# Optimization experiments

Hardware: AMD Instinct MI355X
Metric: run time of the kernel (lower is better)

Reference implementation:

```python
import jax, jax.numpy as jnp
import numpy as np

N_NODES = 50000
N_EDGES = 800000
F_DIM = 64


def setup_inputs() -> dict:
    key = jax.random.key(0)
    ks = jax.random.split(key, 8)
    idx_i = jax.random.randint(ks[0], (N_EDGES,), 0, N_NODES)
    idx_j = jax.random.randint(ks[1], (N_EDGES,), 0, N_NODES)
    px = jax.random.normal(ks[2], (N_NODES, 3, F_DIM), dtype=jnp.float32)
    diff = jax.random.normal(ks[3], (N_EDGES, 3, 1), dtype=jnp.float32)
    s = 1.0 / np.sqrt(F_DIM)
    W_pp = jax.random.normal(ks[4], (F_DIM, F_DIM), dtype=jnp.float32) * s
    W_i = jax.random.normal(ks[5], (F_DIM, F_DIM), dtype=jnp.float32) * s
    W_j = jax.random.normal(ks[6], (F_DIM, F_DIM), dtype=jnp.float32) * s
    W_ii = jax.random.normal(ks[7], (F_DIM, F_DIM), dtype=jnp.float32) * s
    return {"idx_i": idx_i, "idx_j": idx_j, "px": px, "diff": diff,
            "W_pp": W_pp, "W_i": W_i, "W_j": W_j, "W_ii": W_ii}


def reference(idx_i, idx_j, px, diff, W_pp, W_i, W_j, W_ii):
    # PPLayer: bias-free linear on feature dim. px: [N, 3, F]
    px1 = jnp.einsum('nvf,gf->nvg', px, W_pp)
    # PIXLayer: gather endpoints, two bias-free linears, sum. [E, 3, F]
    ix = (jnp.einsum('evf,gf->evg', px1[idx_i], W_i)
          + jnp.einsum('evf,gf->evg', px1[idx_j], W_j))
    # ScaleLayer: elementwise scale by per-edge direction. diff: [E, 3, 1]
    ix = ix * diff
    # IILayer: bias-free linear on edge messages
    ix = jnp.einsum('evf,gf->evg', ix, W_ii)
    # IPLayer: scatter_add back to nodes along dim 0
    px_out = jax.ops.segment_sum(ix, idx_i, num_segments=N_NODES)
    return (px_out, ix)
```

## Files before the change

### kernel.cpp

```cpp
#include <hip/hip_runtime.h>

#define N_NODES 50000
#define N_EDGES 800000
#define F 64
#define NROWS (N_NODES * 3)
#define NPX (N_NODES * 3 * F)

typedef float floatx4 __attribute__((ext_vector_type(4)));

__device__ __forceinline__ unsigned short f2bf(float f) {
  unsigned int u = __float_as_uint(f);
  return (unsigned short)((u + 0x7FFFu + ((u >> 16) & 1u)) >> 16);
}
__device__ __forceinline__ float bf2f(unsigned short h) {
  return __uint_as_float(((unsigned int)h) << 16);
}

__global__ __launch_bounds__(256) void mm64_pair(
    const float* __restrict__ A0, const float* __restrict__ B0, float* __restrict__ O0,
    const float* __restrict__ A1, const float* __restrict__ B1, float* __restrict__ O1) {
  const float* A = (blockIdx.x == 0) ? A0 : A1;
  const float* B = (blockIdx.x == 0) ? B0 : B1;
  float* O = (blockIdx.x == 0) ? O0 : O1;
  __shared__ float As[64][65];
  __shared__ float Bs[64][65];
  int t = threadIdx.x;
  for (int k = 0; k < 16; ++k) {
    int idx = t + 256 * k;
    As[idx >> 6][idx & 63] = A[idx];
    Bs[idx >> 6][idx & 63] = B[idx];
  }
  __syncthreads();
  int g = t >> 2, f0 = (t & 3) * 16;
  float acc[16];
  #pragma unroll
  for (int j = 0; j < 16; ++j) acc[j] = 0.f;
  for (int k = 0; k < 64; ++k) {
    float a = As[g][k];
    #pragma unroll
    for (int j = 0; j < 16; ++j) acc[j] += a * Bs[k][f0 + j];
  }
  for (int j = 0; j < 16; ++j) O[g * 64 + f0 + j] = acc[j];
}

__global__ __launch_bounds__(256) void node_mm(
    const float* __restrict__ px, const float* __restrict__ Bi,
    const float* __restrict__ Bj, float* __restrict__ yi,
    unsigned short* __restrict__ yjb) {
  __shared__ float pxs[64][68];
  __shared__ float Bs[128][68];
  int t = threadIdx.x;
  int r0 = blockIdx.x * 64;
  #pragma unroll
  for (int k = 0; k < 8; ++k) {
    int idx = t + 256 * k;
    int row = idx >> 4, c4 = (idx & 15) * 4;
    const float* src = (row < 64) ? (Bi + row * 64 + c4) : (Bj + (row - 64) * 64 + c4);
    *(float4*)&Bs[row][c4] = *(const float4*)src;
  }
  #pragma unroll
  for (int k = 0; k < 4; ++k) {
    int idx = t + 256 * k;
    int lr = idx >> 4, c4 = (idx & 15) * 4;
    float4 v = make_float4(0.f, 0.f, 0.f, 0.f);
    if (r0 + lr < NROWS) v = *(const float4*)(px + (size_t)(r0 + lr) * 64 + c4);
    *(float4*)&pxs[lr][c4] = v;
  }
  __syncthreads();
  int q = t & 31;
  int rg = t >> 5;
  float acc[8][4];
  #pragma unroll
  for (int r = 0; r < 8; ++r)
    #pragma unroll
    for (int j = 0; j < 4; ++j) acc[r][j] = 0.f;
  #pragma unroll 4
  for (int fc = 0; fc < 16; ++fc) {
    float4 b[4];
    #pragma unroll
    for (int j = 0; j < 4; ++j) b[j] = *(const float4*)&Bs[4 * q + j][fc * 4];
    #pragma unroll
    for (int r = 0; r < 8; ++r) {
      float4 p = *(const float4*)&pxs[rg * 8 + r][fc * 4];
      #pragma unroll
      for (int j = 0; j < 4; ++j)
        acc[r][j] += p.x * b[j].x + p.y * b[j].y + p.z * b[j].z + p.w * b[j].w;
    }
  }
  #pragma unroll
  for (int r = 0; r < 8; ++r) {
    int grow = r0 + rg * 8 + r;
    if (grow >= NROWS) continue;
    if (q < 16) {
      float4 v = make_float4(acc[r][0], acc[r][1], acc[r][2], acc[r][3]);
      *(float4*)(yi + (size_t)grow * 64 + q * 4) = v;
    } else {
      ushort4 h;
      h.x = f2bf(acc[r][0]); h.y = f2bf(acc[r][1]);
      h.z = f2bf(acc[r][2]); h.w = f2bf(acc[r][3]);
      *(ushort4*)(yjb + (size_t)grow * 64 + (q - 16) * 4) = h;
    }
  }
}

__global__ __launch_bounds__(256) void hist_kernel(
    const int* __restrict__ idx_i, int* __restrict__ cnt) {
  int e = blockIdx.x * 256 + threadIdx.x;
  if (e < N_EDGES) atomicAdd(&cnt[idx_i[e]], 1);
}

__global__ __launch_bounds__(1024) void scan_kernel(
    const int* __restrict__ cnt, int* __restrict__ offs, int* __restrict__ cursor) {
  __shared__ int wsum[16];
  __shared__ int s_carry;
  int t = threadIdx.x, w = t >> 6, l = t & 63;
  if (t == 0) { s_carry = 0; offs[0] = 0; }
  __syncthreads();
  for (int base = 0; base < N_NODES; base += 8192) {
    int i0 = base + t * 8;
    int x[8];
    if (i0 + 7 < N_NODES) {
      int4 a = *(const int4*)(cnt + i0);
      int4 b = *(const int4*)(cnt + i0 + 4);
      x[0] = a.x; x[1] = a.y; x[2] = a.z; x[3] = a.w;
      x[4] = b.x; x[5] = b.y; x[6] = b.z; x[7] = b.w;
    } else {
      #pragma unroll
      for (int k = 0; k < 8; ++k) x[k] = (i0 + k < N_NODES) ? cnt[i0 + k] : 0;
    }
    int incl[8];
    int p = 0;
    #pragma unroll
    for (int k = 0; k < 8; ++k) { p += x[k]; incl[k] = p; }
    int tsum = p;
    int ts = tsum;
    #pragma unroll
    for (int off = 1; off < 64; off <<= 1) {
      int y = __shfl_up(ts, off, 64);
      if (l >= off) ts += y;
    }
    if (l == 63) wsum[w] = ts;
    __syncthreads();
    if (t < 16) {
      int ws_ = wsum[t];
      int si = ws_;
      #pragma unroll
      for (int off = 1; off < 16; off <<= 1) {
        int y = __shfl_up(si, off, 16);
        if (t >= off) si += y;
      }
      wsum[t] = si - ws_;
    }
    __syncthreads();
    int basev = s_carry + wsum[w] + (ts - tsum);
    #pragma unroll
    for (int k = 0; k < 8; ++k) {
      int i = i0 + k;
      if (i < N_NODES) {
        int it = basev + incl[k];
        offs[i + 1] = it;
        cursor[i] = it - x[k];
      }
    }
    __syncthreads();
    if (t == 1023) s_carry = basev + tsum;
    __syncthreads();
  }
}

__global__ __launch_bounds__(256) void scatter_kernel(
    const int* __restrict__ idx_i, const int* __restrict__ idx_j,
    const float* __restrict__ diff, int* __restrict__ cursor,
    int* __restrict__ perm, int* __restrict__ pnj, float* __restrict__ pdiff) {
  int e = blockIdx.x * 256 + threadIdx.x;
  if (e < N_EDGES) {
    int pos = atomicAdd(&cursor[idx_i[e]], 1);
    perm[pos] = e;
    pnj[pos] = idx_j[e];
    pdiff[pos * 3 + 0] = diff[e * 3 + 0];
    pdiff[pos * 3 + 1] = diff[e * 3 + 1];
    pdiff[pos * 3 + 2] = diff[e * 3 + 2];
  }
}

__global__ __launch_bounds__(64) void node_edge_kernel(
    const int* __restrict__ offs, const int* __restrict__ perm,
    const int* __restrict__ pnj, const float* __restrict__ pdiff,
    const float* __restrict__ yi, const unsigned short* __restrict__ yjb,
    float* __restrict__ ix_out, float* __restrict__ px_out) {
  int n = blockIdx.x;
  int lane = threadIdx.x;
  int s = lane >> 4;
  int fqs = (lane & 15) * 4;
  int start = offs[n], end = offs[n + 1];
  size_t nbase = (size_t)n * 192 + fqs;

  float4 yiv[3];
  #pragma unroll
  for (int v = 0; v < 3; ++v) yiv[v] = *(const float4*)(yi + nbase + v * 64);

  float4 acc[3];
  float sum_d[3];
  #pragma unroll
  for (int v = 0; v < 3; ++v) {
    acc[v] = make_float4(0.f, 0.f, 0.f, 0.f);
    sum_d[v] = 0.f;
  }

  for (int p = start + s; p < end; p += 4) {
    int e  = perm[p];
    int nj = pnj[p];
    float d[3];
    d[0] = pdiff[p * 3 + 0]; d[1] = pdiff[p * 3 + 1]; d[2] = pdiff[p * 3 + 2];
    const unsigned short* ybase = yjb + (size_t)nj * 192 + fqs;
    ushort4 w[3];
    #pragma unroll
    for (int v = 0; v < 3; ++v) w[v] = *(const ushort4*)(ybase + v * 64);
    float* dst = ix_out + (size_t)e * 192 + fqs;
    #pragma unroll
    for (int v = 0; v < 3; ++v) {
      float4 yv = make_float4(bf2f(w[v].x), bf2f(w[v].y), bf2f(w[v].z), bf2f(w[v].w));
      acc[v].x += d[v] * yv.x; acc[v].y += d[v] * yv.y;
      acc[v].z += d[v] * yv.z; acc[v].w += d[v] * yv.w;
      sum_d[v] += d[v];
      floatx4 r;
      r.x = d[v] * (yiv[v].x + yv.x); r.y = d[v] * (yiv[v].y + yv.y);
      r.z = d[v] * (yiv[v].z + yv.z); r.w = d[v] * (yiv[v].w + yv.w);
      __builtin_nontemporal_store(r, (floatx4*)(dst + v * 64));
    }
  }
  #pragma unroll
  for (int mm = 16; mm < 64; mm <<= 1) {
    #pragma unroll
    for (int v = 0; v < 3; ++v) {
      acc[v].x += __shfl_xor(acc[v].x, mm, 64);
      acc[v].y += __shfl_xor(acc[v].y, mm, 64);
      acc[v].z += __shfl_xor(acc[v].z, mm, 64);
      acc[v].w += __shfl_xor(acc[v].w, mm, 64);
      sum_d[v] += __shfl_xor(sum_d[v], mm, 64);
    }
  }
  if (s == 0) {
    #pragma unroll
    for (int v = 0; v < 3; ++v) {
      float4 o = make_float4(yiv[v].x * sum_d[v] + acc[v].x,
                             yiv[v].y * sum_d[v] + acc[v].y,
                             yiv[v].z * sum_d[v] + acc[v].z,
                             yiv[v].w * sum_d[v] + acc[v].w);
      *(float4*)(px_out + nbase + v * 64) = o;
    }
  }
}

extern "C" void kernel_launch(void* const* d_in, const int* in_sizes, int n_in,
                              void* d_out, int out_size, void* d_ws, size_t ws_size,
                              hipStream_t stream) {
  const int*   idx_i = (const int*)d_in[0];
  const int*   idx_j = (const int*)d_in[1];
  const float* px    = (const float*)d_in[2];
  const float* diff  = (const float*)d_in[3];
  const float* W_pp  = (const float*)d_in[4];
  const float* W_i   = (const float*)d_in[5];
  const float* W_j   = (const float*)d_in[6];
  const float* W_ii  = (const float*)d_in[7];

  float* px_out = (float*)d_out;
  float* ix_out = (float*)d_out + NPX;

  float* ws = (float*)d_ws;
  float* yi = ws;
  unsigned short* yjb = (unsigned short*)(yi + (size_t)NPX);
  float* Ci = (float*)(yjb + (size_t)NPX);
  float* Cj = Ci + 4096;
  float* Bi = Cj + 4096;
  float* Bj = Bi + 4096;
  int* cnt    = (int*)(Bj + 4096);
  int* offs   = cnt + N_NODES;
  int* cursor = offs + N_NODES + 1;
  int* perm   = cursor + N_NODES;
  int* pnj    = perm + N_EDGES;
  float* pdiff = (float*)(pnj + N_EDGES);

  (void)hipMemsetAsync(cnt, 0, N_NODES * sizeof(int), stream);

  mm64_pair<<<2, 256, 0, stream>>>(W_ii, W_i, Ci, W_ii, W_j, Cj);
  mm64_pair<<<2, 256, 0, stream>>>(Ci, W_pp, Bi, Cj, W_pp, Bj);

  node_mm<<<(NROWS + 63) / 64, 256, 0, stream>>>(px, Bi, Bj, yi, yjb);

  hist_kernel<<<(N_EDGES + 255) / 256, 256, 0, stream>>>(idx_i, cnt);
  scan_kernel<<<1, 1024, 0, stream>>>(cnt, offs, cursor);
  scatter_kernel<<<(N_EDGES + 255) / 256, 256, 0, stream>>>(
      idx_i, idx_j, diff, cursor, perm, pnj, pdiff);

  node_edge_kernel<<<N_NODES, 64, 0, stream>>>(offs, perm, pnj, pdiff,
                                               yi, yjb, ix_out, px_out);
}
```

Baseline: 321.6 us.

## Merge small kernels into combined launches and store yi in bf16

Folds the two weight-product launches and the edge histogram into one kernel, and runs the prefix scan on one block of the node matmul launch. This cuts the launch count from seven to four and hides the serial scan behind the matmul blocks. The yi intermediate is now stored as bf16 as well, which halves its write and read traffic. The cost is reduced precision on yi, and the scan now runs on a single 256-thread block, so the serial chain is longer and may be critical.

Measured after the change: 309.5 us. -3.8%, faster.

```diff
diff --git a/kernel.cpp b/kernel.cpp
--- a/kernel.cpp
+++ b/kernel.cpp
@@ -5,6 +5,8 @@
 #define F 64
 #define NROWS (N_NODES * 3)
 #define NPX (N_NODES * 3 * F)
+#define NMM_BLOCKS ((NROWS + 63) / 64)
+#define HIST_BLOCKS ((N_EDGES + 1023) / 1024)
 
 typedef float floatx4 __attribute__((ext_vector_type(4)));
 
@@ -16,19 +18,32 @@
   return __uint_as_float(((unsigned int)h) << 16);
 }
 
-__global__ __launch_bounds__(256) void mm64_pair(
-    const float* __restrict__ A0, const float* __restrict__ B0, float* __restrict__ O0,
-    const float* __restrict__ A1, const float* __restrict__ B1, float* __restrict__ O1) {
-  const float* A = (blockIdx.x == 0) ? A0 : A1;
-  const float* B = (blockIdx.x == 0) ? B0 : B1;
-  float* O = (blockIdx.x == 0) ? O0 : O1;
+__global__ __launch_bounds__(256) void pre_kernel(
+    const float* __restrict__ W_ii, const float* __restrict__ W_i,
+    const float* __restrict__ W_j, const float* __restrict__ W_pp,
+    float* __restrict__ Bi, float* __restrict__ Bj,
+    const int* __restrict__ idx_i, int* __restrict__ cnt) {
   __shared__ float As[64][65];
   __shared__ float Bs[64][65];
+  __shared__ float Ps[64][65];
+  if (blockIdx.x >= 2) {
+    int b = blockIdx.x - 2;
+    int base = b * 1024 + threadIdx.x;
+    #pragma unroll
+    for (int k = 0; k < 4; ++k) {
+      int e = base + k * 256;
+      if (e < N_EDGES) atomicAdd(&cnt[idx_i[e]], 1);
+    }
+    return;
+  }
+  const float* Wx = (blockIdx.x == 0) ? W_i : W_j;
+  float* Out = (blockIdx.x == 0) ? Bi : Bj;
   int t = threadIdx.x;
   for (int k = 0; k < 16; ++k) {
     int idx = t + 256 * k;
-    As[idx >> 6][idx & 63] = A[idx];
-    Bs[idx >> 6][idx & 63] = B[idx];
+    As[idx >> 6][idx & 63] = W_ii[idx];
+    Bs[idx >> 6][idx & 63] = Wx[idx];
+    Ps[idx >> 6][idx & 63] = W_pp[idx];
   }
   __syncthreads();
   int g = t >> 2, f0 = (t & 3) * 16;
@@ -40,17 +55,83 @@
     #pragma unroll
     for (int j = 0; j < 16; ++j) acc[j] += a * Bs[k][f0 + j];
   }
-  for (int j = 0; j < 16; ++j) O[g * 64 + f0 + j] = acc[j];
-}
-
-__global__ __launch_bounds__(256) void node_mm(
+  __syncthreads();
+  #pragma unroll
+  for (int j = 0; j < 16; ++j) As[g][f0 + j] = acc[j];
+  __syncthreads();
+  #pragma unroll
+  for (int j = 0; j < 16; ++j) acc[j] = 0.f;
+  for (int k = 0; k < 64; ++k) {
+    float a = As[g][k];
+    #pragma unroll
+    for (int j = 0; j < 16; ++j) acc[j] += a * Ps[k][f0 + j];
+  }
+  for (int j = 0; j < 16; ++j) Out[g * 64 + f0 + j] = acc[j];
+}
+
+__global__ __launch_bounds__(256) void mm_scan_kernel(
     const float* __restrict__ px, const float* __restrict__ Bi,
-    const float* __restrict__ Bj, float* __restrict__ yi,
-    unsigned short* __restrict__ yjb) {
+    const float* __restrict__ Bj, unsigned short* __restrict__ ybi,
+    unsigned short* __restrict__ ybj,
+    const int* __restrict__ cnt, int* __restrict__ offs,
+    int* __restrict__ cursor) {
   __shared__ float pxs[64][68];
   __shared__ float Bs[128][68];
+  __shared__ int wsum[4];
+  __shared__ int s_carry;
   int t = threadIdx.x;
-  int r0 = blockIdx.x * 64;
+  if (blockIdx.x == 0) {
+    int w = t >> 6, l = t & 63;
+    if (t == 0) { s_carry = 0; offs[0] = 0; }
+    __syncthreads();
+    for (int base = 0; base < N_NODES; base += 2048) {
+      int i0 = base + t * 8;
+      int x[8];
+      if (i0 + 7 < N_NODES) {
+        int4 a = *(const int4*)(cnt + i0);
+        int4 b = *(const int4*)(cnt + i0 + 4);
+        x[0] = a.x; x[1] = a.y; x[2] = a.z; x[3] = a.w;
+        x[4] = b.x; x[5] = b.y; x[6] = b.z; x[7] = b.w;
+      } else {
+        #pragma unroll
+        for (int k = 0; k < 8; ++k) x[k] = (i0 + k < N_NODES) ? cnt[i0 + k] : 0;
+      }
+      int incl[8];
+      int p = 0;
+      #pragma unroll
+      for (int k = 0; k < 8; ++k) { p += x[k]; incl[k] = p; }
+      int tsum = p;
+      int ts = tsum;
+      #pragma unroll
+      for (int off = 1; off < 64; off <<= 1) {
+        int y = __shfl_up(ts, off, 64);
+        if (l >= off) ts += y;
+      }
+      if (l == 63) wsum[w] = ts;
+      __syncthreads();
+      if (t == 0) {
+        int a = 0;
+        #pragma unroll
+        for (int k = 0; k < 4; ++k) { int tmp = wsum[k]; wsum[k] = a; a += tmp; }
+      }
+      __syncthreads();
+      int basev = s_carry + wsum[w] + (ts - tsum);
+      #pragma unroll
+      for (int k = 0; k < 8; ++k) {
+        int i = i0 + k;
+        if (i < N_NODES) {
+          int it = basev + incl[k];
+          offs[i + 1] = it;
+          cursor[i] = it - x[k];
+        }
+      }
+      __syncthreads();
+      if (t == 255) s_carry = basev + tsum;
+      __syncthreads();
+    }
+    return;
+  }
+  int r0 = (blockIdx.x - 1) * 64;
   #pragma unroll
   for (int k = 0; k < 8; ++k) {
     int idx = t + 256 * k;
@@ -91,80 +172,11 @@
   for (int r = 0; r < 8; ++r) {
     int grow = r0 + rg * 8 + r;
     if (grow >= NROWS) continue;
-    if (q < 16) {
-      float4 v = make_float4(acc[r][0], acc[r][1], acc[r][2], acc[r][3]);
-      *(float4*)(yi + (size_t)grow * 64 + q * 4) = v;
-    } else {
-      ushort4 h;
-      h.x = f2bf(acc[r][0]); h.y = f2bf(acc[r][1]);
-      h.z = f2bf(acc[r][2]); h.w = f2bf(acc[r][3]);
-      *(ushort4*)(yjb + (size_t)grow * 64 + (q - 16) * 4) = h;
-    }
-  }
-}
-
-__global__ __launch_bounds__(256) void hist_kernel(
-    const int* __restrict__ idx_i, int* __restrict__ cnt) {
-  int e = blockIdx.x * 256 + threadIdx.x;
-  if (e < N_EDGES) atomicAdd(&cnt[idx_i[e]], 1);
-}
-
-__global__ __launch_bounds__(1024) void scan_kernel(
-    const int* __restrict__ cnt, int* __restrict__ offs, int* __restrict__ cursor) {
-  __shared__ int wsum[16];
-  __shared__ int s_carry;
-  int t = threadIdx.x, w = t >> 6, l = t & 63;
-  if (t == 0) { s_carry = 0; offs[0] = 0; }
-  __syncthreads();
-  for (int base = 0; base < N_NODES; base += 8192) {
-    int i0 = base + t * 8;
-    int x[8];
-    if (i0 + 7 < N_NODES) {
-      int4 a = *(const int4*)(cnt + i0);
-      int4 b = *(const int4*)(cnt + i0 + 4);
-      x[0] = a.x; x[1] = a.y; x[2] = a.z; x[3] = a.w;
-      x[4] = b.x; x[5] = b.y; x[6] = b.z; x[7] = b.w;
-    } else {
-      #pragma unroll
-      for (int k = 0; k < 8; ++k) x[k] = (i0 + k < N_NODES) ? cnt[i0 + k] : 0;
-    }
-    int incl[8];
-    int p = 0;
-    #pragma unroll
-    for (int k = 0; k < 8; ++k) { p += x[k]; incl[k] = p; }
-    int tsum = p;
-    int ts = tsum;
-    #pragma unroll
-    for (int off = 1; off < 64; off <<= 1) {
-      int y = __shfl_up(ts, off, 64);
-      if (l >= off) ts += y;
-    }
-    if (l == 63) wsum[w] = ts;
-    __syncthreads();
-    if (t < 16) {
-      int ws_ = wsum[t];
-      int si = ws_;
-      #pragma unroll
-      for (int off = 1; off < 16; off <<= 1) {
-        int y = __shfl_up(si, off, 16);
-        if (t >= off) si += y;
-      }
-      wsum[t] = si - ws_;
-    }
-    __syncthreads();
-    int basev = s_carry + wsum[w] + (ts - tsum);
-    #pragma unroll
-    for (int k = 0; k < 8; ++k) {
-      int i = i0 + k;
-      if (i < N_NODES) {
-        int it = basev + incl[k];
-        offs[i + 1] = it;
-        cursor[i] = it - x[k];
-      }
-    }
-    __syncthreads();
-    if (t == 1023) s_carry = basev + tsum;
-    __syncthreads();
+    ushort4 h;
+    h.x = f2bf(acc[r][0]); h.y = f2bf(acc[r][1]);
+    h.z = f2bf(acc[r][2]); h.w = f2bf(acc[r][3]);
+    if (q < 16) *(ushort4*)(ybi + (size_t)grow * 64 + q * 4) = h;
+    else        *(ushort4*)(ybj + (size_t)grow * 64 + (q - 16) * 4) = h;
   }
 }
 
@@ -186,7 +198,7 @@
 __global__ __launch_bounds__(64) void node_edge_kernel(
     const int* __restrict__ offs, const int* __restrict__ perm,
     const int* __restrict__ pnj, const float* __restrict__ pdiff,
-    const float* __restrict__ yi, const unsigned short* __restrict__ yjb,
+    const unsigned short* __restrict__ ybi, const unsigned short* __restrict__ ybj,
     float* __restrict__ ix_out, float* __restrict__ px_out) {
   int n = blockIdx.x;
   int lane = threadIdx.x;
@@ -197,7 +209,10 @@
 
   float4 yiv[3];
   #pragma unroll
-  for (int v = 0; v < 3; ++v) yiv[v] = *(const float4*)(yi + nbase + v * 64);
+  for (int v = 0; v < 3; ++v) {
+    ushort4 h = *(const ushort4*)(ybi + nbase + v * 64);
+    yiv[v] = make_float4(bf2f(h.x), bf2f(h.y), bf2f(h.z), bf2f(h.w));
+  }
 
   float4 acc[3];
   float sum_d[3];
@@ -212,7 +227,7 @@
     int nj = pnj[p];
     float d[3];
     d[0] = pdiff[p * 3 + 0]; d[1] = pdiff[p * 3 + 1]; d[2] = pdiff[p * 3 + 2];
-    const unsigned short* ybase = yjb + (size_t)nj * 192 + fqs;
+    const unsigned short* ybase = ybj + (size_t)nj * 192 + fqs;
     ushort4 w[3];
     #pragma unroll
     for (int v = 0; v < 3; ++v) w[v] = *(const ushort4*)(ybase + v * 64);
@@ -267,12 +282,9 @@
   float* px_out = (float*)d_out;
   float* ix_out = (float*)d_out + NPX;
 
-  float* ws = (float*)d_ws;
-  float* yi = ws;
-  unsigned short* yjb = (unsigned short*)(yi + (size_t)NPX);
-  float* Ci = (float*)(yjb + (size_t)NPX);
-  float* Cj = Ci + 4096;
-  float* Bi = Cj + 4096;
+  unsigned short* ybi = (unsigned short*)d_ws;
+  unsigned short* ybj = ybi + (size_t)NPX;
+  float* Bi = (float*)(ybj + (size_t)NPX);
   float* Bj = Bi + 4096;
   int* cnt    = (int*)(Bj + 4096);
   int* offs   = cnt + N_NODES;
@@ -283,16 +295,15 @@
 
   (void)hipMemsetAsync(cnt, 0, N_NODES * sizeof(int), stream);
 
-  mm64_pair<<<2, 256, 0, stream>>>(W_ii, W_i, Ci, W_ii, W_j, Cj);
-  mm64_pair<<<2, 256, 0, stream>>>(Ci, W_pp, Bi, Cj, W_pp, Bj);
-
-  node_mm<<<(NROWS + 63) / 64, 256, 0, stream>>>(px, Bi, Bj, yi, yjb);
-
-  hist_kernel<<<(N_EDGES + 255) / 256, 256, 0, stream>>>(idx_i, cnt);
-  scan_kernel<<<1, 1024, 0, stream>>>(cnt, offs, cursor);
+  pre_kernel<<<2 + HIST_BLOCKS, 256, 0, stream>>>(
+      W_ii, W_i, W_j, W_pp, Bi, Bj, idx_i, cnt);
+
+  mm_scan_kernel<<<1 + NMM_BLOCKS, 256, 0, stream>>>(
+      px, Bi, Bj, ybi, ybj, cnt, offs, cursor);
+
   scatter_kernel<<<(N_EDGES + 255) / 256, 256, 0, stream>>>(
       idx_i, idx_j, diff, cursor, perm, pnj, pdiff);
 
   node_edge_kernel<<<N_NODES, 64, 0, stream>>>(offs, perm, pnj, pdiff,
-                                               yi, yjb, ix_out, px_out);
-}
+                                               ybi, ybj, ix_out, px_out);
+}
```
